# Kernel tuning notes

Measured on AMD Instinct MI355X. Metric: run time of the kernel, lower is better.

The kernel has to match this reference:

```python
import jax, jax.numpy as jnp
import numpy as np

B, S, D = 2, 2048, 1024
H = 16
HD = D // H  # 64


def setup_inputs() -> dict:
    key = jax.random.key(0)
    k1, k2, k3, k4, k5, k6 = jax.random.split(key, 6)
    hidden_states = jax.random.normal(k1, (B, S, D), dtype=jnp.float32)
    attention_mask = jax.random.randint(k2, (B, S), 0, 2, dtype=jnp.int32)
    scale = 1.0 / np.sqrt(D)
    Wq = jax.random.normal(k3, (D, D), dtype=jnp.float32) * scale
    bq = jax.random.normal(k4, (D,), dtype=jnp.float32) * 0.02
    Wk = jax.random.normal(k5, (D, D), dtype=jnp.float32) * scale
    bk = jax.random.normal(k6, (D,), dtype=jnp.float32) * 0.02
    return {"hidden_states": hidden_states, "attention_mask": attention_mask,
            "Wq": Wq, "bq": bq, "Wk": Wk, "bk": bk}


def _split_heads(x):
    # [B, S, D] -> [B, H, S, HD]
    b, s, _ = x.shape
    return x.reshape(b, s, H, HD).transpose(0, 2, 1, 3)


def reference(hidden_states, attention_mask, Wq, bq, Wk, bk):
    dh = jnp.sqrt(jnp.float32(HD))
    q = _split_heads(hidden_states @ Wq + bq)            # [B,H,S,HD]
    k = _split_heads(hidden_states @ Wk + bk)            # [B,H,S,HD]
    v = q + k                                            # value = Q + K
    k_t = -jax.nn.log_sigmoid(-k)                        # negate the logsigmoid(-K) transform
    scores = jnp.einsum('bhqd,bhkd->bhqk', q, k_t) / dh  # [B,H,S,S]
    # mask applied on the QUERY axis (dim 2), broadcast over key axis (faithful to source)
    mask = (attention_mask[:, None, :, None] == 0)       # [B,1,S,1]
    scores = jnp.where(mask, jnp.float32(-10000.0), scores)
    probs = jax.nn.softmax(scores, axis=-1)              # dropout: eval mode (identity)
    ctx = jnp.einsum('bhqk,bhkd->bhqd', probs, v)        # [B,H,S,HD]
    ctx = ctx.transpose(0, 2, 1, 3).reshape(B, S, D)
    return ctx
```

## Files before the change

kernel.cpp:

```cpp
#include <hip/hip_runtime.h>
#include <hip/hip_bf16.h>

#define B_ 2
#define S_ 2048
#define D_ 1024
#define H_ 16
#define HD_ 64

typedef __attribute__((ext_vector_type(8))) short short8;
typedef __attribute__((ext_vector_type(4))) short short4v;
typedef __attribute__((ext_vector_type(4))) float float4v;

typedef const __attribute__((address_space(1))) void* gas_ptr;
typedef __attribute__((address_space(3))) void* las_ptr;

static __device__ inline void gl_lds16(const void* g, void* l) {
  __builtin_amdgcn_global_load_lds((gas_ptr)g, (las_ptr)l, 16, 0, 0);
}

static __device__ inline float b2f(__hip_bfloat16 h) { return __bfloat162float(h); }

static __device__ inline short f2bs(float x) {
  __hip_bfloat16 h = __float2bfloat16(x);
  union { __hip_bfloat16 h; short s; } u; u.h = h; return u.s;
}
static __device__ inline float bs2f(short s) {
  union { short s; __hip_bfloat16 h; } u; u.s = s; return __bfloat162float(u.h);
}
static __device__ inline short4v pk4(float a, float b, float c, float d) {
  union { __hip_bfloat162 h[2]; short4v s; } u;
  u.h[0] = __float22bfloat162_rn(float2{a, b});
  u.h[1] = __float22bfloat162_rn(float2{c, d});
  return u.s;
}

static __device__ inline float4v mfma32(short8 a, short8 b, float4v c) {
  return __builtin_amdgcn_mfma_f32_16x16x32_bf16(a, b, c, 0, 0, 0);
}
static __device__ inline float4v mfma16(short4v a, short4v b, float4v c) {
  return __builtin_amdgcn_mfma_f32_16x16x16bf16_1k(a, b, c, 0, 0, 0);
}

__global__ __launch_bounds__(256) void cvt(
    const float* __restrict__ in, __hip_bfloat16* __restrict__ out) {
  const size_t i = ((size_t)blockIdx.x * 256 + threadIdx.x) * 8;
  const float4v a0 = ((const float4v*)(in + i))[0];
  const float4v a1 = ((const float4v*)(in + i))[1];
  short8 s;
#pragma unroll
  for (int j = 0; j < 4; ++j) { s[j] = f2bs(a0[j]); s[4 + j] = f2bs(a1[j]); }
  *(short8*)(out + i) = s;
}

__global__ __launch_bounds__(256) void pre(
    const float* __restrict__ Wq, const float* __restrict__ Wk,
    __hip_bfloat16* __restrict__ Wqt, __hip_bfloat16* __restrict__ Wkt) {
  const float* W = blockIdx.z ? Wk : Wq;
  __hip_bfloat16* Wt = blockIdx.z ? Wkt : Wqt;
  __shared__ float t[64][65];
  const int n0 = blockIdx.x * 64, k0 = blockIdx.y * 64;
  const int c = threadIdx.x & 63, r0 = threadIdx.x >> 6;
  for (int i = 0; i < 16; ++i) {
    const int r = i * 4 + r0;
    t[c][r] = W[(size_t)(k0 + r) * D_ + n0 + c];
  }
  __syncthreads();
  for (int i = 0; i < 16; ++i) {
    const int rr = i * 4 + r0;
    Wt[(size_t)(n0 + rr) * D_ + k0 + c] = __float2bfloat16(t[rr][c]);
  }
}

__global__ __launch_bounds__(512, 2) void gemm_fused(
    const __hip_bfloat16* __restrict__ hsb,
    const __hip_bfloat16* __restrict__ Wqt, const __hip_bfloat16* __restrict__ Wkt,
    const float* __restrict__ bq, const float* __restrict__ bk,
    __hip_bfloat16* __restrict__ q_out, __hip_bfloat16* __restrict__ kt_out,
    __hip_bfloat16* __restrict__ vT) {
  const int id = blockIdx.x;
  const int mt = (id & 7) * 4 + ((id >> 3) & 3);
  const int nt = id >> 5;
  const int n0 = nt * 128, m0 = mt * 128;
  __shared__ __hip_bfloat16 As[2][128 * 32];
  __shared__ __hip_bfloat16 Bq[2][128 * 32];
  __shared__ __hip_bfloat16 Bk[2][128 * 32];
  const int tid = threadIdx.x, wid = tid >> 6, lane = tid & 63;
  const int wm = (wid >> 1) * 32, wn = (wid & 1) * 64;
  const int l15 = lane & 15, l4 = lane >> 4;
  const float4v zz = {0.f, 0.f, 0.f, 0.f};
  float4v accq[2][4], acck[2][4];
  for (int i = 0; i < 2; ++i)
    for (int j = 0; j < 4; ++j) { accq[i][j] = zz; acck[i][j] = zz; }
  const int lrow = wid * 16 + (lane >> 2);
  const int lk8 = (((lane & 3) ^ ((lane >> 3) & 3)) * 8);
  {
    gl_lds16(hsb + (size_t)(m0 + lrow) * D_ + lk8, As[0] + wid * 512);
    gl_lds16(Wqt + (size_t)(n0 + lrow) * D_ + lk8, Bq[0] + wid * 512);
    gl_lds16(Wkt + (size_t)(n0 + lrow) * D_ + lk8, Bk[0] + wid * 512);
  }
  int p = 0;
  for (int kb = 0; kb < 32; ++kb) {
    __syncthreads();
    if (kb < 31) {
      const int kc = (kb + 1) * 32 + lk8;
      gl_lds16(hsb + (size_t)(m0 + lrow) * D_ + kc, As[p ^ 1] + wid * 512);
      gl_lds16(Wqt + (size_t)(n0 + lrow) * D_ + kc, Bq[p ^ 1] + wid * 512);
      gl_lds16(Wkt + (size_t)(n0 + lrow) * D_ + kc, Bk[p ^ 1] + wid * 512);
    }
    short8 af[2], bfq[4], bfk[4];
    const int fo = ((l4 ^ ((l15 >> 1) & 3)) * 8);
    for (int rt = 0; rt < 2; ++rt)
      af[rt] = *(const short8*)(As[p] + (wm + rt * 16 + l15) * 32 + fo);
    for (int ct = 0; ct < 4; ++ct) {
      bfq[ct] = *(const short8*)(Bq[p] + (wn + ct * 16 + l15) * 32 + fo);
      bfk[ct] = *(const short8*)(Bk[p] + (wn + ct * 16 + l15) * 32 + fo);
    }
    for (int rt = 0; rt < 2; ++rt)
      for (int ct = 0; ct < 4; ++ct) {
        accq[rt][ct] = mfma32(af[rt], bfq[ct], accq[rt][ct]);
        acck[rt][ct] = mfma32(af[rt], bfk[ct], acck[rt][ct]);
      }
    p ^= 1;
  }
  float bvq[4], bvk[4];
  for (int ct = 0; ct < 4; ++ct) {
    bvq[ct] = bq[n0 + wn + ct * 16 + l15];
    bvk[ct] = bk[n0 + wn + ct * 16 + l15];
  }
  for (int rt = 0; rt < 2; ++rt)
    for (int ct = 0; ct < 4; ++ct) {
      const int col = n0 + wn + ct * 16 + l15;
      const int h = col >> 6, d = col & 63;
      const int rowb = m0 + wm + rt * 16 + l4 * 4;
      short4v vv;
      for (int r = 0; r < 4; ++r) {
        const int row = rowb + r;
        const float qv = accq[rt][ct][r] + bvq[ct];
        const float kv = acck[rt][ct][r] + bvk[ct];
        const float sp = fmaxf(kv, 0.f) + __logf(1.f + __expf(-fabsf(kv)));
        q_out[(size_t)row * D_ + col] = __float2bfloat16(qv);
        kt_out[(size_t)row * D_ + col] = __float2bfloat16(sp);
        vv[r] = f2bs(qv + kv);
      }
      const int b = rowb >> 11, s = rowb & 2047;
      const int sw = (s & ~63) | (((s >> 4) & 3) << 2) | (((s >> 2) & 3) << 4);
      *(short4v*)(vT + ((size_t)(b * H_ + h) * HD_ + d) * S_ + sw) = vv;
    }
}

__global__ __launch_bounds__(256, 2) void attn(
    const __hip_bfloat16* __restrict__ qb, const __hip_bfloat16* __restrict__ ktb,
    const __hip_bfloat16* __restrict__ vT, const int* __restrict__ mask,
    float* __restrict__ out) {
  __shared__ short smem[32768];
  const int id = blockIdx.x;
  const int xcd = id & 7;
  const int rest = id >> 3;
  const int q0 = (rest & 15) * 128;
  const int hb = (rest >> 4) * 8 + xcd;
  const int h = hb >> 1, b = hb & 1;
  const int tid = threadIdx.x, wid = tid >> 6, lane = tid & 63;
  const int l15 = lane & 15, l4 = lane >> 4;
  const __hip_bfloat16* qh = qb + (size_t)b * S_ * D_ + h * HD_;
  const __hip_bfloat16* kh = ktb + (size_t)b * S_ * D_ + h * HD_;
  const __hip_bfloat16* vh = vT + (size_t)(b * H_ + h) * HD_ * S_;
  const int srow = tid >> 2;
  const int b0 = tid & 3;
  const int ssw = ((srow & 1) << 2) | ((srow >> 1) & 3);
  const int w0 = srow * 64 + ((b0 ^ ssw) * 8);
  const int w1 = srow * 64 + (((b0 + 4) ^ ssw) * 8);

  const int qlA = wid * 32 + l15, qlB = qlA + 16;
  const int qrA = q0 + qlA, qrB = q0 + qlB;
  const float SC = 0.125f * 1.44269504f;
  const float mqA = (mask[b * S_ + qrA] != 0) ? SC : 0.f;
  const float mqB = (mask[b * S_ + qrB] != 0) ? SC : 0.f;
  const short8 rA0 = *(const short8*)(qh + (size_t)qrA * D_ + l4 * 8);
  const short8 rA1 = *(const short8*)(qh + (size_t)qrA * D_ + 32 + l4 * 8);
  const short8 rB0 = *(const short8*)(qh + (size_t)qrB * D_ + l4 * 8);
  const short8 rB1 = *(const short8*)(qh + (size_t)qrB * D_ + 32 + l4 * 8);
  short8 bqA0, bqA1, bqB0, bqB1;
  for (int j = 0; j < 8; ++j) {
    bqA0[j] = f2bs(bs2f(rA0[j]) * mqA);
    bqA1[j] = f2bs(bs2f(rA1[j]) * mqA);
    bqB0[j] = f2bs(bs2f(rB0[j]) * mqB);
    bqB1[j] = f2bs(bs2f(rB1[j]) * mqB);
  }

  const int lsw = ((l15 & 1) << 2) | ((l15 >> 1) & 3);
  const int ak0off = l15 * 64 + ((l4 ^ lsw) * 8);
  const int ak1off = l15 * 64 + (((l4 + 4) ^ lsw) * 8);
  const int vb0off = ((2 * l4) ^ lsw) * 8;
  const int vb1off = ((2 * l4 + 1) ^ lsw) * 8;

  const float4v zz = {0.f, 0.f, 0.f, 0.f};
  float4v oaccA[4] = {zz, zz, zz, zz};
  float4v oaccB[4] = {zz, zz, zz, zz};
  float lsumA = 0.f, lsumB = 0.f;

  short8 gk0[2], gk1[2], gv0[2], gv1[2];
#pragma unroll
  for (int u = 0; u < 2; ++u) {
    gk0[u] = *(const short8*)(kh + (size_t)(u * 64 + srow) * D_ + b0 * 8);
    gk1[u] = *(const short8*)(kh + (size_t)(u * 64 + srow) * D_ + b0 * 8 + 32);
    gv0[u] = *(const short8*)(vh + (size_t)srow * S_ + u * 64 + b0 * 8);
    gv1[u] = *(const short8*)(vh + (size_t)srow * S_ + u * 64 + b0 * 8 + 32);
  }

  int p = 0;
  for (int c = 0; c < 16; ++c) {
    short* bufp = smem + p * 16384;
#pragma unroll
    for (int u = 0; u < 2; ++u) {
      *(short8*)(bufp + u * 4096 + w0) = gk0[u];
      *(short8*)(bufp + u * 4096 + w1) = gk1[u];
      *(short8*)(bufp + 8192 + u * 4096 + w0) = gv0[u];
      *(short8*)(bufp + 8192 + u * 4096 + w1) = gv1[u];
    }
    __syncthreads();
    if (c < 15) {
      const int kb = (c + 1) * 128;
#pragma unroll
      for (int u = 0; u < 2; ++u) {
        gk0[u] = *(const short8*)(kh + (size_t)(kb + u * 64 + srow) * D_ + b0 * 8);
        gk1[u] = *(const short8*)(kh + (size_t)(kb + u * 64 + srow) * D_ + b0 * 8 + 32);
        gv0[u] = *(const short8*)(vh + (size_t)srow * S_ + kb + u * 64 + b0 * 8);
        gv1[u] = *(const short8*)(vh + (size_t)srow * S_ + kb + u * 64 + b0 * 8 + 32);
      }
    }
#pragma unroll
    for (int u = 0; u < 2; ++u) {
      const short* kbase = bufp + u * 4096;
      const short* vbase = bufp + 8192 + u * 4096;
      short4v pA[4], pB[4];
#pragma unroll
      for (int t = 0; t < 4; ++t) {
        const short8 ak0 = *(const short8*)(kbase + t * 1024 + ak0off);
        const short8 ak1 = *(const short8*)(kbase + t * 1024 + ak1off);
        float4v cA = zz, cB = zz;
        cA = mfma32(ak0, bqA0, cA);
        cA = mfma32(ak1, bqA1, cA);
        cB = mfma32(ak0, bqB0, cB);
        cB = mfma32(ak1, bqB1, cB);
        float eA[4], eB[4];
#pragma unroll
        for (int r = 0; r < 4; ++r) {
          eA[r] = __builtin_amdgcn_exp2f(cA[r]); lsumA += eA[r];
          eB[r] = __builtin_amdgcn_exp2f(cB[r]); lsumB += eB[r];
        }
        pA[t] = pk4(eA[0], eA[1], eA[2], eA[3]);
        pB[t] = pk4(eB[0], eB[1], eB[2], eB[3]);
      }
#pragma unroll
      for (int dt = 0; dt < 4; ++dt) {
        const int rb = (dt * 16 + l15) * 64;
        const short8 av0 = *(const short8*)(vbase + rb + vb0off);
        const short8 av1 = *(const short8*)(vbase + rb + vb1off);
        const short4v a0 = {av0[0], av0[1], av0[2], av0[3]};
        const short4v a1 = {av0[4], av0[5], av0[6], av0[7]};
        const short4v a2 = {av1[0], av1[1], av1[2], av1[3]};
        const short4v a3 = {av1[4], av1[5], av1[6], av1[7]};
        oaccA[dt] = mfma16(a0, pA[0], oaccA[dt]);
        oaccB[dt] = mfma16(a0, pB[0], oaccB[dt]);
        oaccA[dt] = mfma16(a1, pA[1], oaccA[dt]);
        oaccB[dt] = mfma16(a1, pB[1], oaccB[dt]);
        oaccA[dt] = mfma16(a2, pA[2], oaccA[dt]);
        oaccB[dt] = mfma16(a2, pB[2], oaccB[dt]);
        oaccA[dt] = mfma16(a3, pA[3], oaccA[dt]);
        oaccB[dt] = mfma16(a3, pB[3], oaccB[dt]);
      }
    }
    p ^= 1;
  }
  float lA = lsumA + __shfl_xor(lsumA, 16); lA += __shfl_xor(lA, 32);
  float lB = lsumB + __shfl_xor(lsumB, 16); lB += __shfl_xor(lB, 32);
  __syncthreads();
  float* mbuf = (float*)smem;
  float* mlb = (float*)smem + 128 * 68;
#pragma unroll
  for (int dt = 0; dt < 4; ++dt)
#pragma unroll
    for (int r = 0; r < 4; ++r) {
      mbuf[qlA * 68 + dt * 16 + l4 * 4 + r] = oaccA[dt][r];
      mbuf[qlB * 68 + dt * 16 + l4 * 4 + r] = oaccB[dt][r];
    }
  if (l4 == 0) { mlb[qlA] = lA; mlb[qlB] = lB; }
  __syncthreads();
  const int qq = tid >> 1;
  const int dg = (tid & 1) * 32;
  const float li = 1.f / mlb[qq];
  float* orow = out + (size_t)(b * S_ + q0 + qq) * D_ + h * HD_ + dg;
#pragma unroll
  for (int i = 0; i < 8; ++i) {
    float4v v = *(const float4v*)&mbuf[qq * 68 + dg + i * 4];
#pragma unroll
    for (int r = 0; r < 4; ++r) v[r] *= li;
    *(float4v*)(orow + i * 4) = v;
  }
}

extern "C" void kernel_launch(void* const* d_in, const int* in_sizes, int n_in,
                              void* d_out, int out_size, void* d_ws, size_t ws_size,
                              hipStream_t stream) {
  const float* hs = (const float*)d_in[0];
  const int* mask = (const int*)d_in[1];
  const float* Wq = (const float*)d_in[2];
  const float* bq = (const float*)d_in[3];
  const float* Wk = (const float*)d_in[4];
  const float* bk = (const float*)d_in[5];
  float* out = (float*)d_out;
  char* ws = (char*)d_ws;
  const size_t MB = 1u << 20;
  __hip_bfloat16* q_b = (__hip_bfloat16*)(ws + 0 * MB);
  __hip_bfloat16* k_b = (__hip_bfloat16*)(ws + 8 * MB);
  __hip_bfloat16* vT  = (__hip_bfloat16*)(ws + 16 * MB);
  __hip_bfloat16* Wqt = (__hip_bfloat16*)(ws + 24 * MB);
  __hip_bfloat16* Wkt = (__hip_bfloat16*)(ws + 26 * MB);
  __hip_bfloat16* hsb = (__hip_bfloat16*)(ws + 28 * MB);

  cvt<<<dim3(2048), 256, 0, stream>>>(hs, hsb);
  pre<<<dim3(16, 16, 2), 256, 0, stream>>>(Wq, Wk, Wqt, Wkt);
  gemm_fused<<<dim3(256), 512, 0, stream>>>(hsb, Wqt, Wkt, bq, bk, q_b, k_b, vT);
  attn<<<dim3(512), 256, 0, stream>>>(q_b, k_b, vT, mask, out);
}
```

Baseline: 161.4 us.

## Merge conversion kernels and retile QK projection GEMM to 64x128 blocks

Fuses the hidden-state bf16 conversion and weight transpose kernels into one launch, removing one kernel launch and its tail. The projection GEMM now uses 256-thread blocks with 64-row M tiles and 512 blocks instead of 512-thread blocks with 128-row tiles. Each warp issues two B loads per operand to fill the 128-column tiles, so more blocks are available to spread across CUs. The trade-off is less reuse of the weight tiles across rows per block.

Measured after the change: 158.6 us. Within noise of the previous version (-1.7%).

```diff
diff --git a/kernel.cpp b/kernel.cpp
--- a/kernel.cpp
+++ b/kernel.cpp
@@ -18,8 +18,6 @@
   __builtin_amdgcn_global_load_lds((gas_ptr)g, (las_ptr)l, 16, 0, 0);
 }
 
-static __device__ inline float b2f(__hip_bfloat16 h) { return __bfloat162float(h); }
-
 static __device__ inline short f2bs(float x) {
   __hip_bfloat16 h = __float2bfloat16(x);
   union { __hip_bfloat16 h; short s; } u; u.h = h; return u.s;
@@ -41,24 +39,26 @@
   return __builtin_amdgcn_mfma_f32_16x16x16bf16_1k(a, b, c, 0, 0, 0);
 }
 
-__global__ __launch_bounds__(256) void cvt(
-    const float* __restrict__ in, __hip_bfloat16* __restrict__ out) {
-  const size_t i = ((size_t)blockIdx.x * 256 + threadIdx.x) * 8;
-  const float4v a0 = ((const float4v*)(in + i))[0];
-  const float4v a1 = ((const float4v*)(in + i))[1];
-  short8 s;
-#pragma unroll
-  for (int j = 0; j < 4; ++j) { s[j] = f2bs(a0[j]); s[4 + j] = f2bs(a1[j]); }
-  *(short8*)(out + i) = s;
-}
-
-__global__ __launch_bounds__(256) void pre(
+__global__ __launch_bounds__(256) void prep(
+    const float* __restrict__ hs, __hip_bfloat16* __restrict__ hsb,
     const float* __restrict__ Wq, const float* __restrict__ Wk,
     __hip_bfloat16* __restrict__ Wqt, __hip_bfloat16* __restrict__ Wkt) {
-  const float* W = blockIdx.z ? Wk : Wq;
-  __hip_bfloat16* Wt = blockIdx.z ? Wkt : Wqt;
   __shared__ float t[64][65];
-  const int n0 = blockIdx.x * 64, k0 = blockIdx.y * 64;
+  const int id = blockIdx.x;
+  if (id < 2048) {
+    const size_t i = ((size_t)id * 256 + threadIdx.x) * 8;
+    const float4v a0 = ((const float4v*)(hs + i))[0];
+    const float4v a1 = ((const float4v*)(hs + i))[1];
+    short8 s;
+#pragma unroll
+    for (int j = 0; j < 4; ++j) { s[j] = f2bs(a0[j]); s[4 + j] = f2bs(a1[j]); }
+    *(short8*)(hsb + i) = s;
+    return;
+  }
+  const int bid = id - 2048;
+  const float* W = (bid >> 8) ? Wk : Wq;
+  __hip_bfloat16* Wt = (bid >> 8) ? Wkt : Wqt;
+  const int n0 = (bid & 15) * 64, k0 = ((bid >> 4) & 15) * 64;
   const int c = threadIdx.x & 63, r0 = threadIdx.x >> 6;
   for (int i = 0; i < 16; ++i) {
     const int r = i * 4 + r0;
@@ -71,17 +71,17 @@
   }
 }
 
-__global__ __launch_bounds__(512, 2) void gemm_fused(
+__global__ __launch_bounds__(256, 2) void gemm_fused(
     const __hip_bfloat16* __restrict__ hsb,
     const __hip_bfloat16* __restrict__ Wqt, const __hip_bfloat16* __restrict__ Wkt,
     const float* __restrict__ bq, const float* __restrict__ bk,
     __hip_bfloat16* __restrict__ q_out, __hip_bfloat16* __restrict__ kt_out,
     __hip_bfloat16* __restrict__ vT) {
   const int id = blockIdx.x;
-  const int mt = (id & 7) * 4 + ((id >> 3) & 3);
-  const int nt = id >> 5;
-  const int n0 = nt * 128, m0 = mt * 128;
-  __shared__ __hip_bfloat16 As[2][128 * 32];
+  const int mt = (id & 7) * 8 + ((id >> 3) & 7);
+  const int nt = id >> 6;
+  const int n0 = nt * 128, m0 = mt * 64;
+  __shared__ __hip_bfloat16 As[2][64 * 32];
   __shared__ __hip_bfloat16 Bq[2][128 * 32];
   __shared__ __hip_bfloat16 Bk[2][128 * 32];
   const int tid = threadIdx.x, wid = tid >> 6, lane = tid & 63;
@@ -96,7 +96,9 @@
   {
     gl_lds16(hsb + (size_t)(m0 + lrow) * D_ + lk8, As[0] + wid * 512);
     gl_lds16(Wqt + (size_t)(n0 + lrow) * D_ + lk8, Bq[0] + wid * 512);
+    gl_lds16(Wqt + (size_t)(n0 + 64 + lrow) * D_ + lk8, Bq[0] + 2048 + wid * 512);
     gl_lds16(Wkt + (size_t)(n0 + lrow) * D_ + lk8, Bk[0] + wid * 512);
+    gl_lds16(Wkt + (size_t)(n0 + 64 + lrow) * D_ + lk8, Bk[0] + 2048 + wid * 512);
   }
   int p = 0;
   for (int kb = 0; kb < 32; ++kb) {
@@ -105,7 +107,9 @@
       const int kc = (kb + 1) * 32 + lk8;
       gl_lds16(hsb + (size_t)(m0 + lrow) * D_ + kc, As[p ^ 1] + wid * 512);
       gl_lds16(Wqt + (size_t)(n0 + lrow) * D_ + kc, Bq[p ^ 1] + wid * 512);
+      gl_lds16(Wqt + (size_t)(n0 + 64 + lrow) * D_ + kc, Bq[p ^ 1] + 2048 + wid * 512);
       gl_lds16(Wkt + (size_t)(n0 + lrow) * D_ + kc, Bk[p ^ 1] + wid * 512);
+      gl_lds16(Wkt + (size_t)(n0 + 64 + lrow) * D_ + kc, Bk[p ^ 1] + 2048 + wid * 512);
     }
     short8 af[2], bfq[4], bfk[4];
     const int fo = ((l4 ^ ((l15 >> 1) & 3)) * 8);
@@ -318,8 +322,7 @@
   __hip_bfloat16* Wkt = (__hip_bfloat16*)(ws + 26 * MB);
   __hip_bfloat16* hsb = (__hip_bfloat16*)(ws + 28 * MB);
 
-  cvt<<<dim3(2048), 256, 0, stream>>>(hs, hsb);
-  pre<<<dim3(16, 16, 2), 256, 0, stream>>>(Wq, Wk, Wqt, Wkt);
-  gemm_fused<<<dim3(256), 512, 0, stream>>>(hsb, Wqt, Wkt, bq, bk, q_b, k_b, vT);
+  prep<<<dim3(2560), 256, 0, stream>>>(hs, hsb, Wq, Wk, Wqt, Wkt);
+  gemm_fused<<<dim3(512), 256, 0, stream>>>(hsb, Wqt, Wkt, bq, bk, q_b, k_b, vT);
   attn<<<dim3(512), 256, 0, stream>>>(q_b, k_b, vT, mask, out);
 }
```
